# Performance work log

Hardware: AMD Instinct MI355X
Metric: run time of the kernel (lower is better)

Reference implementation:

```python
import jax, jax.numpy as jnp
import numpy as np

B, T = 4, 8
H, W = 120, 160
NON_SEM = 4
CAT = 16
MAP_CH = NON_SEM + CAT          # 20 map channels
FEAT_CH = 2 * NON_SEM + CAT     # 24 feature channels
RES = 5.0                       # cm per map cell
GLOBAL_M, LOCAL_M = 960, 240    # map_size/resolution, and /downscale
M2 = LOCAL_M * LOCAL_M
HFOV = 79.0
CAM_H_CM = 88.0
VISION_CM = 100 * RES           # vision_range cells -> cm
AGENT_R2 = 2.0 ** 2
EXPLORE_R2 = 3.0 ** 2
FX = W / (2.0 * float(np.tan(np.deg2rad(HFOV) / 2.0)))
FY = FX
CX, CY = W / 2.0, H / 2.0

LOCAL_POSE0 = jnp.array([LOCAL_M * RES / 2, LOCAL_M * RES / 2, 0.0], jnp.float32)
GLOBAL_POSE0 = jnp.array([GLOBAL_M * RES / 2, GLOBAL_M * RES / 2, 0.0], jnp.float32)
OFF = (GLOBAL_M - LOCAL_M) // 2
BOUNDS0 = jnp.array([OFF, OFF + LOCAL_M, OFF, OFF + LOCAL_M], jnp.int32)
ORIGINS0 = jnp.array([OFF * RES, OFF * RES, 0.0], jnp.float32)


def _splat1(flat, w):  # scatter-add scalar weights into the flattened local grid
    return jnp.zeros((M2,), jnp.float32).at[flat].add(w)


def _splatC(flat, vals):  # vals [C, N] -> [C, M2]
    return jnp.zeros((vals.shape[0], M2), jnp.float32).at[:, flat].add(vals)


def _step(carry, xs):
    lmap, gmap, lpose, gpose, bounds, origins = carry
    obs, delta, cam_T, done, upd = xs
    doneb = done != 0
    # per-env reset on episode end (init_map_and_pose_for_env)
    lmap = jnp.where(doneb[:, None, None, None], 0.0, lmap)
    gmap = jnp.where(doneb[:, None, None, None], 0.0, gmap)
    lpose = jnp.where(doneb[:, None], LOCAL_POSE0, lpose)
    gpose = jnp.where(doneb[:, None], GLOBAL_POSE0, gpose)
    bounds = jnp.where(doneb[:, None], BOUNDS0, bounds)
    origins = jnp.where(doneb[:, None], ORIGINS0, origins)

    # dead-reckoning pose update (delta in agent frame)
    th = jnp.deg2rad(lpose[:, 2])
    dx = delta[:, 0] * jnp.cos(th) - delta[:, 1] * jnp.sin(th)
    dy = delta[:, 0] * jnp.sin(th) + delta[:, 1] * jnp.cos(th)
    lpose = lpose + jnp.stack([dx, dy, delta[:, 2]], -1)

    # depth -> camera-frame point cloud (cm)
    depth = obs[:, 3] * 400.0 + 50.0  # [B,H,W]
    sem = obs[:, NON_SEM:]            # [B,CAT,H,W]
    uu = (jnp.arange(W, dtype=jnp.float32) - CX)[None, None, :]
    vv = (CY - jnp.arange(H, dtype=jnp.float32))[None, :, None]
    pts = jnp.stack([uu * depth / FX, vv * depth / FY, depth, jnp.ones_like(depth)], -1)
    pts = jnp.einsum('bij,bhwj->bhwi', cam_T, pts)  # camera extrinsics
    x_f, y_l, z_u = pts[..., 2], -pts[..., 0], pts[..., 1] + CAM_H_CM

    # agent frame -> local map frame
    th2 = jnp.deg2rad(lpose[:, 2])[:, None, None]
    wx = lpose[:, 0][:, None, None] + x_f * jnp.cos(th2) - y_l * jnp.sin(th2)
    wy = lpose[:, 1][:, None, None] + x_f * jnp.sin(th2) + y_l * jnp.cos(th2)
    ix = jnp.floor(wx / RES).astype(jnp.int32)
    iy = jnp.floor(wy / RES).astype(jnp.int32)
    valid = (depth > 25.0) & (depth < VISION_CM) & (ix >= 0) & (ix < LOCAL_M) & (iy >= 0) & (iy < LOCAL_M)
    flat = (jnp.clip(iy, 0, LOCAL_M - 1) * LOCAL_M + jnp.clip(ix, 0, LOCAL_M - 1)).reshape(B, -1)
    vm = valid.reshape(B, -1).astype(jnp.float32)
    obst_w = vm * ((z_u > 25.0) & (z_u < 150.0)).reshape(B, -1).astype(jnp.float32)

    exp_grid = jax.vmap(_splat1)(flat, vm).reshape(B, LOCAL_M, LOCAL_M)
    obst_grid = jax.vmap(_splat1)(flat, obst_w).reshape(B, LOCAL_M, LOCAL_M)
    sem_grid = jax.vmap(_splatC)(flat, sem.reshape(B, CAT, -1) * vm[:, None, :]).reshape(B, CAT, LOCAL_M, LOCAL_M)

    # agent location / been-close disks
    g = jnp.arange(LOCAL_M, dtype=jnp.float32)
    dxg = g[None, None, :] - (lpose[:, 0] / RES)[:, None, None]
    dyg = g[None, :, None] - (lpose[:, 1] / RES)[:, None, None]
    d2 = dxg * dxg + dyg * dyg
    agent = (d2 <= AGENT_R2).astype(jnp.float32)
    close = (d2 <= EXPLORE_R2).astype(jnp.float32)

    lmap = jnp.concatenate([
        jnp.maximum(lmap[:, 0], jnp.clip(obst_grid, 0.0, 1.0))[:, None],
        jnp.maximum(lmap[:, 1], jnp.clip(exp_grid, 0.0, 1.0))[:, None],
        agent[:, None],
        jnp.maximum(lmap[:, 3], close)[:, None],
        jnp.maximum(lmap[:, NON_SEM:], jnp.clip(sem_grid, 0.0, 1.0)),
    ], axis=1)

    # fuse local window into global map for envs flagged for update
    y1, x1 = bounds[:, 0], bounds[:, 2]
    crop = jax.vmap(lambda gm, y, x: jax.lax.dynamic_slice(gm, (0, y, x), (MAP_CH, LOCAL_M, LOCAL_M)))(gmap, y1, x1)
    updb = (upd != 0)[:, None, None, None]
    fused = jnp.where(updb, jnp.maximum(crop, lmap), crop)
    gmap = jax.vmap(lambda gm, c, y, x: jax.lax.dynamic_update_slice(gm, c, (0, y, x)))(gmap, fused, y1, x1)
    gpose = jnp.where((upd != 0)[:, None], lpose + origins, gpose)

    feats = jnp.concatenate([lmap[:, :NON_SEM], fused[:, :NON_SEM], lmap[:, NON_SEM:]], axis=1)
    return (lmap, gmap, lpose, gpose, bounds, origins), (feats, lpose, gpose, bounds, origins)


def _forward(obs_seq, pose_delta, cam_poses, init_local_map, init_global_map,
             init_local_pose, init_global_pose, init_origins,
             done_flags, update_flags, init_bounds):
    xs = (obs_seq.swapaxes(0, 1), pose_delta.swapaxes(0, 1), cam_poses.swapaxes(0, 1),
          done_flags.swapaxes(0, 1), update_flags.swapaxes(0, 1))
    carry0 = (init_local_map, init_global_map, init_local_pose, init_global_pose, init_bounds, init_origins)
    carry, ys = jax.lax.scan(_step, carry0, xs)
    feats, lp, gp, bnds, orgs = ys
    return (feats.swapaxes(0, 1), carry[0], carry[1], lp.swapaxes(0, 1), gp.swapaxes(0, 1),
            bnds.swapaxes(0, 1), orgs.swapaxes(0, 1))


def setup_inputs() -> dict:
    key = jax.random.key(0)
    ks = jax.random.split(key, 5)
    obs_seq = jax.random.uniform(ks[0], (B, T, MAP_CH, H, W), jnp.float32)
    pose_delta = jax.random.normal(ks[1], (B, T, 3), jnp.float32) * jnp.array([10.0, 2.0, 5.0], jnp.float32)
    cam_poses = jnp.eye(4, dtype=jnp.float32)[None, None] + 0.02 * jax.random.normal(ks[2], (B, T, 4, 4), jnp.float32)
    done_flags = jax.random.randint(ks[3], (B, T), 0, 2, jnp.int32)
    update_flags = jax.random.randint(ks[4], (B, T), 0, 2, jnp.int32)
    return {
        'obs_seq': obs_seq,
        'pose_delta': pose_delta,
        'done_flags': done_flags,
        'update_flags': update_flags,
        'cam_poses': cam_poses,
        'init_local_map': jnp.zeros((B, MAP_CH, LOCAL_M, LOCAL_M), jnp.float32),
        'init_global_map': jnp.zeros((B, MAP_CH, GLOBAL_M, GLOBAL_M), jnp.float32),
        'init_local_pose': jnp.tile(LOCAL_POSE0[None], (B, 1)),
        'init_global_pose': jnp.tile(GLOBAL_POSE0[None], (B, 1)),
        'init_bounds': jnp.tile(BOUNDS0[None], (B, 1)),
        'init_origins': jnp.tile(ORIGINS0[None], (B, 1)),
    }


def reference(obs_seq, pose_delta, done_flags, update_flags, cam_poses,
              init_local_map, init_global_map, init_local_pose, init_global_pose,
              init_bounds, init_origins):
    return _forward(obs_seq, pose_delta, cam_poses, init_local_map, init_global_map,
                    init_local_pose, init_global_pose, init_origins,
                    done_flags, update_flags, init_bounds)
```

## Files before the change

### kernel.cpp

```cpp
#include <hip/hip_runtime.h>
#include <math.h>

#define Bn 4
#define Tn 8
#define Hn 120
#define Wn 160
#define HWn (Hn * Wn)
#define NON_SEMn 4
#define CATn 16
#define MAP_CHn 20
#define FEAT_CHn 24
#define LOCAL_Mn 240
#define GLOBAL_Mn 960
#define M2n (LOCAL_Mn * LOCAL_Mn)
#define BMn (Bn * M2n)
#define TBMn (Tn * Bn * M2n)
#define Pn (Tn * Bn * HWn)
#define NTILE_SCAN 1800
#define PROJ_BLKS ((Pn + 255) / 256)
#define UPD2_BLKS ((2 * BMn + 255) / 256)
#define GMAP_BLKS ((Bn * MAP_CHn * GLOBAL_Mn * GLOBAL_Mn / 4 + 255) / 256)

#define DEG2RADf ((float)0.017453292519943295)

typedef float vf4 __attribute__((ext_vector_type(4)));

#define OUT_FEATS 0
#define OUT_LMAP  44236800
#define OUT_GMAP  48844800
#define OUT_LP    122572800
#define OUT_GP    122572896
#define OUT_BNDS  122572992
#define OUT_ORGS  122573120

#define WS_CNTR   96
#define WS_REC2   128
#define WS_BSUM   (WS_REC2 + 2 * TBMn)
#define WS_CELL   (WS_BSUM + 2048)
#define WS_RECB   (WS_CELL + Pn)

__device__ __forceinline__ void pose_upto(const float* __restrict__ pose_delta,
                                          const int* __restrict__ done_flags,
                                          const float* __restrict__ init_lpose,
                                          int b, int tt,
                                          float& lx, float& ly, float& lz) {
#pragma clang fp contract(off)
    lx = init_lpose[b * 3 + 0];
    ly = init_lpose[b * 3 + 1];
    lz = init_lpose[b * 3 + 2];
    for (int t = 0; t <= tt; t++) {
        if (done_flags[b * Tn + t]) { lx = 600.0f; ly = 600.0f; lz = 0.0f; }
        float th = lz * DEG2RADf;
        float c = cosf(th), s = sinf(th);
        float d0 = pose_delta[(b * Tn + t) * 3 + 0];
        float d1 = pose_delta[(b * Tn + t) * 3 + 1];
        float d2 = pose_delta[(b * Tn + t) * 3 + 2];
        lx = lx + (d0 * c - d1 * s);
        ly = ly + (d0 * s + d1 * c);
        lz = lz + d2;
    }
}

__global__ void __launch_bounds__(256)
project_kernel(const float* __restrict__ obs,
               const float* __restrict__ cam,
               const float* __restrict__ pose_delta,
               const int* __restrict__ done_flags,
               const int* __restrict__ upd_flags,
               const float* __restrict__ init_lpose,
               const float* __restrict__ init_gpose,
               const int* __restrict__ init_bounds,
               const float* __restrict__ init_origins,
               uint2* __restrict__ rec2,
               int* __restrict__ cellid,
               float* __restrict__ out_lp,
               float* __restrict__ out_gp,
               float* __restrict__ out_bnds,
               float* __restrict__ out_orgs,
               float fx) {
#pragma clang fp contract(off)
    if (blockIdx.x == 0 && threadIdx.x < Bn) {
        int b = threadIdx.x;
        float lx = init_lpose[b * 3 + 0], ly = init_lpose[b * 3 + 1], lz = init_lpose[b * 3 + 2];
        float gx = init_gpose[b * 3 + 0], gy = init_gpose[b * 3 + 1], gz = init_gpose[b * 3 + 2];
        int b0 = init_bounds[b * 4 + 0], b1 = init_bounds[b * 4 + 1];
        int b2i = init_bounds[b * 4 + 2], b3 = init_bounds[b * 4 + 3];
        float ox = init_origins[b * 3 + 0], oy = init_origins[b * 3 + 1], oz = init_origins[b * 3 + 2];
        for (int t = 0; t < Tn; t++) {
            int done = done_flags[b * Tn + t];
            int upd  = upd_flags[b * Tn + t];
            if (done) {
                lx = 600.0f; ly = 600.0f; lz = 0.0f;
                gx = 2400.0f; gy = 2400.0f; gz = 0.0f;
                b0 = 360; b1 = 600; b2i = 360; b3 = 600;
                ox = 1800.0f; oy = 1800.0f; oz = 0.0f;
            }
            float th = lz * DEG2RADf;
            float c = cosf(th), sn = sinf(th);
            float d0 = pose_delta[(b * Tn + t) * 3 + 0];
            float d1 = pose_delta[(b * Tn + t) * 3 + 1];
            float d2 = pose_delta[(b * Tn + t) * 3 + 2];
            lx = lx + (d0 * c - d1 * sn);
            ly = ly + (d0 * sn + d1 * c);
            lz = lz + d2;
            if (upd) { gx = lx + ox; gy = ly + oy; gz = lz + oz; }
            out_lp[(b * Tn + t) * 3 + 0] = lx;
            out_lp[(b * Tn + t) * 3 + 1] = ly;
            out_lp[(b * Tn + t) * 3 + 2] = lz;
            out_gp[(b * Tn + t) * 3 + 0] = gx;
            out_gp[(b * Tn + t) * 3 + 1] = gy;
            out_gp[(b * Tn + t) * 3 + 2] = gz;
            out_bnds[(b * Tn + t) * 4 + 0] = (float)b0;
            out_bnds[(b * Tn + t) * 4 + 1] = (float)b1;
            out_bnds[(b * Tn + t) * 4 + 2] = (float)b2i;
            out_bnds[(b * Tn + t) * 4 + 3] = (float)b3;
            out_orgs[(b * Tn + t) * 3 + 0] = ox;
            out_orgs[(b * Tn + t) * 3 + 1] = oy;
            out_orgs[(b * Tn + t) * 3 + 2] = oz;
        }
    }

    int g = blockIdx.x * 256 + threadIdx.x;
    if (g >= Pn) return;
    int p = g % HWn;
    int tb = g / HWn;
    int b = tb % Bn;
    int t = tb / Bn;
    int h = p / Wn, w = p % Wn;
    const float* ob = obs + (size_t)((b * Tn + t) * MAP_CHn) * HWn;
    float depth = ob[3 * HWn + p] * 400.0f + 50.0f;
    float u = (float)w - 80.0f;
    float v = 60.0f - (float)h;
    float px = u * depth / fx;
    float py = v * depth / fx;
    float pz = depth;
    const float* Tm = cam + (size_t)(b * Tn + t) * 16;
    float X = ((Tm[0] * px + Tm[1] * py) + Tm[2] * pz) + Tm[3];
    float Y = ((Tm[4] * px + Tm[5] * py) + Tm[6] * pz) + Tm[7];
    float Z = ((Tm[8] * px + Tm[9] * py) + Tm[10] * pz) + Tm[11];
    float x_f = Z;
    float y_l = -X;
    float z_u = Y + 88.0f;
    float lx, ly, lz;
    pose_upto(pose_delta, done_flags, init_lpose, b, t, lx, ly, lz);
    float th2 = lz * DEG2RADf;
    float c2 = cosf(th2), s2 = sinf(th2);
    float wx = (lx + x_f * c2) - y_l * s2;
    float wy = (ly + x_f * s2) + y_l * c2;
    int ix = (int)floorf(wx / 5.0f);
    int iy = (int)floorf(wy / 5.0f);
    bool valid = (depth > 25.0f) && (depth < 500.0f) &&
                 (ix >= 0) && (ix < LOCAL_Mn) && (iy >= 0) && (iy < LOCAL_Mn);
    int cell = -1;
    if (valid) {
        cell = (t * Bn + b) * M2n + iy * LOCAL_Mn + ix;
        unsigned addv = 1u + ((z_u > 25.0f && z_u < 150.0f) ? 65536u : 0u);
        atomicAdd(&rec2[cell].x, addv);
    }
    cellid[g] = cell;
}

__global__ void scan1_kernel(uint2* __restrict__ rec2,
                             unsigned* __restrict__ bsum,
                             unsigned* __restrict__ cntr) {
    __shared__ unsigned s[256];
    int tid = threadIdx.x;
    int base = blockIdx.x * 1024 + tid * 4;
    unsigned v0 = rec2[base].x & 0xFFFFu, v1 = rec2[base + 1].x & 0xFFFFu;
    unsigned v2 = rec2[base + 2].x & 0xFFFFu, v3 = rec2[base + 3].x & 0xFFFFu;
    unsigned tsum = v0 + v1 + v2 + v3;
    s[tid] = tsum;
    __syncthreads();
    for (int d = 1; d < 256; d <<= 1) {
        unsigned a = (tid >= d) ? s[tid - d] : 0u;
        __syncthreads();
        s[tid] += a;
        __syncthreads();
    }
    unsigned excl = s[tid] - tsum;
    if (tid == 255) bsum[blockIdx.x] = atomicAdd(cntr, s[255]);
    rec2[base].y     = excl;
    rec2[base + 1].y = excl + v0;
    rec2[base + 2].y = excl + v0 + v1;
    rec2[base + 3].y = excl + v0 + v1 + v2;
}

__global__ void scatter_copy_kernel(const float* __restrict__ obs,
                                    const int* __restrict__ cellid,
                                    const unsigned* __restrict__ bsum,
                                    uint2* __restrict__ rec2,
                                    float* __restrict__ recb) {
    int g = blockIdx.x * blockDim.x + threadIdx.x;
    if (g >= Pn) return;
    int c = cellid[g];
    if (c < 0) return;
    int p = g % HWn;
    int tb = g / HWn;
    int b = tb % Bn;
    int t = tb / Bn;
    const float* ob = obs + (size_t)((b * Tn + t) * MAP_CHn) * HWn;
    vf4 r[4];
#pragma unroll
    for (int q = 0; q < 4; q++) {
        r[q].x = ob[(size_t)(NON_SEMn + 4 * q + 0) * HWn + p];
        r[q].y = ob[(size_t)(NON_SEMn + 4 * q + 1) * HWn + p];
        r[q].z = ob[(size_t)(NON_SEMn + 4 * q + 2) * HWn + p];
        r[q].w = ob[(size_t)(NON_SEMn + 4 * q + 3) * HWn + p];
    }
    unsigned pos = bsum[c >> 10] + atomicAdd(&rec2[c].y, 1u);
    vf4* rp = (vf4*)(recb + (size_t)pos * CATn);
#pragma unroll
    for (int q = 0; q < 4; q++) rp[q] = r[q];
}

template <int Q>
__device__ __forceinline__ void update_half(
        int b, int j,
        const uint2* __restrict__ rec2,
        const unsigned* __restrict__ bsum,
        const float* __restrict__ recb,
        const int* __restrict__ done_flags,
        const int* __restrict__ upd_flags,
        const float* __restrict__ pose_delta,
        const float* __restrict__ init_lpose,
        const float* __restrict__ init_lmap,
        const float* __restrict__ init_gmap,
        int y1, int x1,
        float* __restrict__ out_feats,
        float* __restrict__ out_lmap,
        float* __restrict__ out_gmap) {
#pragma clang fp contract(off)
    constexpr int CH0 = Q ? 12 : 0;
    constexpr int NCH = Q ? 8 : 12;
    int y = j / LOCAL_Mn, x = j % LOCAL_Mn;

    float lm[NCH], cr[NCH];
#pragma unroll
    for (int i = 0; i < NCH; i++)
        lm[i] = __builtin_nontemporal_load(init_lmap + ((size_t)(b * MAP_CHn + CH0 + i)) * M2n + j);
#pragma unroll
    for (int i = 0; i < NCH; i++)
        cr[i] = __builtin_nontemporal_load(
            init_gmap + ((size_t)(b * MAP_CHn + CH0 + i) * GLOBAL_Mn + (y1 + y)) * GLOBAL_Mn + (x1 + x));

    uint2 rc8[Tn];
#pragma unroll
    for (int t = 0; t < Tn; t++) rc8[t] = rec2[(t * Bn + b) * M2n + j];
    unsigned st8[Tn];
#pragma unroll
    for (int t = 0; t < Tn; t++) {
        unsigned n = rc8[t].x & 0xFFFFu;
        st8[t] = bsum[((t * Bn + b) * M2n + j) >> 10] + rc8[t].y - n;
    }

    float lx = 0.0f, ly = 0.0f, lz = 0.0f;
    if (Q == 0) {
        lx = init_lpose[b * 3 + 0];
        ly = init_lpose[b * 3 + 1];
        lz = init_lpose[b * 3 + 2];
    }

    for (int t = 0; t < Tn; t++) {
        int done = done_flags[b * Tn + t];
        int upd  = upd_flags[b * Tn + t];
        if (done) {
#pragma unroll
            for (int i = 0; i < NCH; i++) { lm[i] = 0.0f; cr[i] = 0.0f; }
        }
        unsigned n = rc8[t].x & 0xFFFFu;

        if (Q == 0) {
            if (done) { lx = 600.0f; ly = 600.0f; lz = 0.0f; }
            float th = lz * DEG2RADf;
            float c = cosf(th), sn = sinf(th);
            float d0 = pose_delta[(b * Tn + t) * 3 + 0];
            float d1 = pose_delta[(b * Tn + t) * 3 + 1];
            float d2p = pose_delta[(b * Tn + t) * 3 + 2];
            lx = lx + (d0 * c - d1 * sn);
            ly = ly + (d0 * sn + d1 * c);
            lz = lz + d2p;
            float dxg = (float)x - lx / 5.0f;
            float dyg = (float)y - ly / 5.0f;
            float d2 = dxg * dxg + dyg * dyg;
            lm[0] = fmaxf(lm[0], (rc8[t].x >> 16) ? 1.0f : 0.0f);
            lm[1] = fmaxf(lm[1], n ? 1.0f : 0.0f);
            lm[2] = (d2 <= 4.0f) ? 1.0f : 0.0f;
            lm[3] = fmaxf(lm[3], (d2 <= 9.0f) ? 1.0f : 0.0f);
        }

        if (n) {
            float sem[8];
#pragma unroll
            for (int c = 0; c < 8; c++) sem[c] = 0.0f;
            const vf4* rp = (const vf4*)(recb + (size_t)st8[t] * CATn) + (Q ? 2 : 0);
            for (unsigned k = 0; k < n; k++) {
                vf4 ra = rp[0], rb = rp[1];
                rp += 4;
                sem[0] += ra.x; sem[1] += ra.y; sem[2] += ra.z; sem[3] += ra.w;
                sem[4] += rb.x; sem[5] += rb.y; sem[6] += rb.z; sem[7] += rb.w;
            }
            constexpr int L0 = Q ? 0 : 4;
#pragma unroll
            for (int c = 0; c < 8; c++)
                lm[L0 + c] = fmaxf(lm[L0 + c], fminf(fmaxf(sem[c], 0.0f), 1.0f));
        }
        if (upd) {
#pragma unroll
            for (int i = 0; i < NCH; i++) cr[i] = fmaxf(cr[i], lm[i]);
        }

        size_t fb = ((size_t)(b * Tn + t) * FEAT_CHn) * M2n + j;
        if (Q == 0) {
#pragma unroll
            for (int i = 0; i < 4; i++)
                __builtin_nontemporal_store(lm[i], out_feats + fb + (size_t)i * M2n);
#pragma unroll
            for (int i = 0; i < 4; i++)
                __builtin_nontemporal_store(cr[i], out_feats + fb + (size_t)(4 + i) * M2n);
#pragma unroll
            for (int i = 0; i < 8; i++)
                __builtin_nontemporal_store(lm[4 + i], out_feats + fb + (size_t)(8 + i) * M2n);
        } else {
#pragma unroll
            for (int i = 0; i < 8; i++)
                __builtin_nontemporal_store(lm[i], out_feats + fb + (size_t)(16 + i) * M2n);
        }
    }

#pragma unroll
    for (int i = 0; i < NCH; i++)
        __builtin_nontemporal_store(lm[i], out_lmap + ((size_t)(b * MAP_CHn + CH0 + i)) * M2n + j);
#pragma unroll
    for (int i = 0; i < NCH; i++)
        __builtin_nontemporal_store(
            cr[i], out_gmap + ((size_t)(b * MAP_CHn + CH0 + i) * GLOBAL_Mn + (y1 + y)) * GLOBAL_Mn + (x1 + x));
}

__global__ void __launch_bounds__(256)
mega_kernel(const uint2* __restrict__ rec2,
            const unsigned* __restrict__ bsum,
            const float* __restrict__ recb,
            const int* __restrict__ done_flags,
            const int* __restrict__ upd_flags,
            const float* __restrict__ pose_delta,
            const float* __restrict__ init_lpose,
            const float* __restrict__ init_lmap,
            const float* __restrict__ init_gmap,
            const int* __restrict__ init_bounds,
            float* __restrict__ out_feats,
            float* __restrict__ out_lmap,
            float* __restrict__ out_gmap) {
    if (blockIdx.x >= UPD2_BLKS) {
        size_t i4 = (size_t)(blockIdx.x - UPD2_BLKS) * 256 + threadIdx.x;
        const size_t total4 = (size_t)Bn * MAP_CHn * GLOBAL_Mn * GLOBAL_Mn / 4;
        if (i4 >= total4) return;
        size_t f = i4 * 4;
        int gx = (int)(f % GLOBAL_Mn);
        size_t r = f / GLOBAL_Mn;
        int gy = (int)(r % GLOBAL_Mn);
        size_t bc = r / GLOBAL_Mn;
        int b = (int)(bc / MAP_CHn);
        int y1 = init_bounds[b * 4 + 0];
        int x1 = init_bounds[b * 4 + 2];
        if (gy >= y1 && gy < y1 + LOCAL_Mn && gx >= x1 && gx < x1 + LOCAL_Mn) return;
        bool anyd = false;
        for (int t = 0; t < Tn; t++) anyd |= (done_flags[b * Tn + t] != 0);
        vf4 v;
        if (anyd) {
            v = (vf4)(0.0f);
        } else {
            v = __builtin_nontemporal_load((const vf4*)(init_gmap + f));
        }
        __builtin_nontemporal_store(v, (vf4*)(out_gmap + f));
        return;
    }

    int idx = blockIdx.x * 256 + threadIdx.x;
    int q = idx / BMn;
    int cid = idx - q * BMn;
    int b = cid / M2n, j = cid % M2n;
    int y1 = init_bounds[b * 4 + 0];
    int x1 = init_bounds[b * 4 + 2];
    if (q == 0)
        update_half<0>(b, j, rec2, bsum, recb, done_flags, upd_flags,
                       pose_delta, init_lpose, init_lmap, init_gmap,
                       y1, x1, out_feats, out_lmap, out_gmap);
    else
        update_half<1>(b, j, rec2, bsum, recb, done_flags, upd_flags,
                       pose_delta, init_lpose, init_lmap, init_gmap,
                       y1, x1, out_feats, out_lmap, out_gmap);
}

extern "C" void kernel_launch(void* const* d_in, const int* in_sizes, int n_in,
                              void* d_out, int out_size, void* d_ws, size_t ws_size,
                              hipStream_t stream) {
    const float* obs        = (const float*)d_in[0];
    const float* pose_delta = (const float*)d_in[1];
    const int*   done_flags = (const int*)d_in[2];
    const int*   upd_flags  = (const int*)d_in[3];
    const float* cam_poses  = (const float*)d_in[4];
    const float* init_lmap  = (const float*)d_in[5];
    const float* init_gmap  = (const float*)d_in[6];
    const float* init_lpose = (const float*)d_in[7];
    const float* init_gpose = (const float*)d_in[8];
    const int*   init_bnds  = (const int*)d_in[9];
    const float* init_orgs  = (const float*)d_in[10];

    float* out = (float*)d_out;
    float* ws  = (float*)d_ws;

    unsigned* cntr   = (unsigned*)(ws + WS_CNTR);
    uint2*    rec2   = (uint2*)(ws + WS_REC2);
    unsigned* bsum   = (unsigned*)(ws + WS_BSUM);
    int*      cellid = (int*)(ws + WS_CELL);
    float*    recb   = ws + WS_RECB;

    float fx = (float)(160.0 / (2.0 * tan(79.0 * M_PI / 180.0 / 2.0)));

    (void)hipMemsetAsync(ws + WS_CNTR, 0,
                         (size_t)(32 + 2 * TBMn) * sizeof(float), stream);

    project_kernel<<<PROJ_BLKS, 256, 0, stream>>>(
        obs, cam_poses, pose_delta, done_flags, upd_flags,
        init_lpose, init_gpose, init_bnds, init_orgs,
        rec2, cellid,
        out + OUT_LP, out + OUT_GP, out + OUT_BNDS, out + OUT_ORGS, fx);

    scan1_kernel<<<NTILE_SCAN, 256, 0, stream>>>(rec2, bsum, cntr);

    scatter_copy_kernel<<<PROJ_BLKS, 256, 0, stream>>>(
        obs, cellid, bsum, rec2, recb);

    mega_kernel<<<UPD2_BLKS + GMAP_BLKS, 256, 0, stream>>>(
        rec2, bsum, recb, done_flags, upd_flags, pose_delta, init_lpose,
        init_lmap, init_gmap, init_bnds,
        out + OUT_FEATS, out + OUT_LMAP, out + OUT_GMAP);
}
```

Before: 792.4 us.

## Split global-map copy across scatter and mega kernels; software-pipeline sem accumulation

Half of the global-map background copy now runs as extra blocks in scatter_copy_kernel, overlapping with the scatter work; the other half stays in mega_kernel. The semantic accumulation loop is software-pipelined so the next record is loaded before the current one is summed. The goal is better use of memory bandwidth across kernels, since the scatter kernel is latency-bound while the copy is bandwidth-bound. The cost is a larger launch for scatter_copy_kernel, and the two halves now compete for bandwidth with different phases.

```diff
diff --git a/kernel.cpp b/kernel.cpp
--- a/kernel.cpp
+++ b/kernel.cpp
@@ -19,7 +19,9 @@
 #define NTILE_SCAN 1800
 #define PROJ_BLKS ((Pn + 255) / 256)
 #define UPD2_BLKS ((2 * BMn + 255) / 256)
-#define GMAP_BLKS ((Bn * MAP_CHn * GLOBAL_Mn * GLOBAL_Mn / 4 + 255) / 256)
+#define GMAP_TOT4 ((size_t)Bn * MAP_CHn * GLOBAL_Mn * GLOBAL_Mn / 4)
+#define GMAP_HALF4 (GMAP_TOT4 / 2)
+#define GMAP_HBLKS ((int)((GMAP_HALF4 + 255) / 256))
 
 #define DEG2RADf ((float)0.017453292519943295)
 
@@ -59,6 +61,31 @@
         ly = ly + (d0 * s + d1 * c);
         lz = lz + d2;
     }
+}
+
+__device__ __forceinline__ void gmap_copy_i4(size_t i4,
+                                             const int* __restrict__ init_bounds,
+                                             const int* __restrict__ done_flags,
+                                             const float* __restrict__ init_gmap,
+                                             float* __restrict__ out_gmap) {
+    size_t f = i4 * 4;
+    int gx = (int)(f % GLOBAL_Mn);
+    size_t r = f / GLOBAL_Mn;
+    int gy = (int)(r % GLOBAL_Mn);
+    size_t bc = r / GLOBAL_Mn;
+    int b = (int)(bc / MAP_CHn);
+    int y1 = init_bounds[b * 4 + 0];
+    int x1 = init_bounds[b * 4 + 2];
+    if (gy >= y1 && gy < y1 + LOCAL_Mn && gx >= x1 && gx < x1 + LOCAL_Mn) return;
+    bool anyd = false;
+    for (int t = 0; t < Tn; t++) anyd |= (done_flags[b * Tn + t] != 0);
+    vf4 v;
+    if (anyd) {
+        v = (vf4)(0.0f);
+    } else {
+        v = __builtin_nontemporal_load((const vf4*)(init_gmap + f));
+    }
+    __builtin_nontemporal_store(v, (vf4*)(out_gmap + f));
 }
 
 __global__ void __launch_bounds__(256)
@@ -185,12 +212,23 @@
     rec2[base + 3].y = excl + v0 + v1 + v2;
 }
 
-__global__ void scatter_copy_kernel(const float* __restrict__ obs,
-                                    const int* __restrict__ cellid,
-                                    const unsigned* __restrict__ bsum,
-                                    uint2* __restrict__ rec2,
-                                    float* __restrict__ recb) {
-    int g = blockIdx.x * blockDim.x + threadIdx.x;
+__global__ void __launch_bounds__(256)
+scatter_copy_kernel(const float* __restrict__ obs,
+                    const int* __restrict__ cellid,
+                    const unsigned* __restrict__ bsum,
+                    uint2* __restrict__ rec2,
+                    float* __restrict__ recb,
+                    const int* __restrict__ init_bounds,
+                    const int* __restrict__ done_flags,
+                    const float* __restrict__ init_gmap,
+                    float* __restrict__ out_gmap) {
+    if (blockIdx.x >= PROJ_BLKS) {
+        size_t i4 = (size_t)(blockIdx.x - PROJ_BLKS) * 256 + threadIdx.x;
+        if (i4 >= GMAP_HALF4) return;
+        gmap_copy_i4(i4, init_bounds, done_flags, init_gmap, out_gmap);
+        return;
+    }
+    int g = blockIdx.x * 256 + threadIdx.x;
     if (g >= Pn) return;
     int c = cellid[g];
     if (c < 0) return;
@@ -293,12 +331,16 @@
 #pragma unroll
             for (int c = 0; c < 8; c++) sem[c] = 0.0f;
             const vf4* rp = (const vf4*)(recb + (size_t)st8[t] * CATn) + (Q ? 2 : 0);
-            for (unsigned k = 0; k < n; k++) {
-                vf4 ra = rp[0], rb = rp[1];
+            vf4 a0 = rp[0], a1 = rp[1];
+            for (unsigned k = 1; k < n; k++) {
                 rp += 4;
-                sem[0] += ra.x; sem[1] += ra.y; sem[2] += ra.z; sem[3] += ra.w;
-                sem[4] += rb.x; sem[5] += rb.y; sem[6] += rb.z; sem[7] += rb.w;
+                vf4 b0 = rp[0], b1 = rp[1];
+                sem[0] += a0.x; sem[1] += a0.y; sem[2] += a0.z; sem[3] += a0.w;
+                sem[4] += a1.x; sem[5] += a1.y; sem[6] += a1.z; sem[7] += a1.w;
+                a0 = b0; a1 = b1;
             }
+            sem[0] += a0.x; sem[1] += a0.y; sem[2] += a0.z; sem[3] += a0.w;
+            sem[4] += a1.x; sem[5] += a1.y; sem[6] += a1.z; sem[7] += a1.w;
             constexpr int L0 = Q ? 0 : 4;
 #pragma unroll
             for (int c = 0; c < 8; c++)
@@ -351,27 +393,9 @@
             float* __restrict__ out_lmap,
             float* __restrict__ out_gmap) {
     if (blockIdx.x >= UPD2_BLKS) {
-        size_t i4 = (size_t)(blockIdx.x - UPD2_BLKS) * 256 + threadIdx.x;
-        const size_t total4 = (size_t)Bn * MAP_CHn * GLOBAL_Mn * GLOBAL_Mn / 4;
-        if (i4 >= total4) return;
-        size_t f = i4 * 4;
-        int gx = (int)(f % GLOBAL_Mn);
-        size_t r = f / GLOBAL_Mn;
-        int gy = (int)(r % GLOBAL_Mn);
-        size_t bc = r / GLOBAL_Mn;
-        int b = (int)(bc / MAP_CHn);
-        int y1 = init_bounds[b * 4 + 0];
-        int x1 = init_bounds[b * 4 + 2];
-        if (gy >= y1 && gy < y1 + LOCAL_Mn && gx >= x1 && gx < x1 + LOCAL_Mn) return;
-        bool anyd = false;
-        for (int t = 0; t < Tn; t++) anyd |= (done_flags[b * Tn + t] != 0);
-        vf4 v;
-        if (anyd) {
-            v = (vf4)(0.0f);
-        } else {
-            v = __builtin_nontemporal_load((const vf4*)(init_gmap + f));
-        }
-        __builtin_nontemporal_store(v, (vf4*)(out_gmap + f));
+        size_t i4 = GMAP_HALF4 + (size_t)(blockIdx.x - UPD2_BLKS) * 256 + threadIdx.x;
+        if (i4 >= GMAP_TOT4) return;
+        gmap_copy_i4(i4, init_bounds, done_flags, init_gmap, out_gmap);
         return;
     }
 
@@ -428,10 +452,11 @@
 
     scan1_kernel<<<NTILE_SCAN, 256, 0, stream>>>(rec2, bsum, cntr);
 
-    scatter_copy_kernel<<<PROJ_BLKS, 256, 0, stream>>>(
-        obs, cellid, bsum, rec2, recb);
-
-    mega_kernel<<<UPD2_BLKS + GMAP_BLKS, 256, 0, stream>>>(
+    scatter_copy_kernel<<<PROJ_BLKS + GMAP_HBLKS, 256, 0, stream>>>(
+        obs, cellid, bsum, rec2, recb,
+        init_bnds, done_flags, init_gmap, out + OUT_GMAP);
+
+    mega_kernel<<<UPD2_BLKS + GMAP_HBLKS, 256, 0, stream>>>(
         rec2, bsum, recb, done_flags, upd_flags, pose_delta, init_lpose,
         init_lmap, init_gmap, init_bnds,
         out + OUT_FEATS, out + OUT_LMAP, out + OUT_GMAP);
```

Result: no change. 787.1 us (-0.7%).
